# Kernel optimization log

Measured on AMD Instinct MI355X. Metric: run time of the kernel, lower is better.

Reference implementation:

```python
import jax, jax.numpy as jnp
import numpy as np

B, DIM, SEQ = 8, 256, 16384
K, RED = 3, 3
HID = DIM // RED          # 85
PAD, STRIDE = 1, 1
EPS = 1e-5                # BatchNorm eps (inference-mode BN with running stats)


def setup_inputs() -> dict:
    key = jax.random.key(0)
    ks = jax.random.split(key, 9)
    return {
        "x": jax.random.normal(ks[0], (B, DIM, SEQ), jnp.float32),
        "w1": jax.random.normal(ks[1], (HID, DIM), jnp.float32) * 0.05,
        "bn_gamma": jax.random.uniform(ks[2], (HID,), jnp.float32, 0.5, 1.5),
        "bn_beta": jax.random.normal(ks[3], (HID,), jnp.float32) * 0.1,
        "bn_mean": jax.random.normal(ks[4], (HID,), jnp.float32) * 0.1,
        "bn_var": jax.random.uniform(ks[5], (HID,), jnp.float32, 0.5, 1.5),
        "w2": jax.random.normal(ks[6], (DIM * K, HID), jnp.float32) * 0.05,
        "b2": jax.random.normal(ks[7], (DIM * K,), jnp.float32) * 0.05,
        "bias": jax.random.normal(ks[8], (DIM,), jnp.float32) * 0.05,
    }


def reference(x, w1, bn_gamma, bn_beta, bn_mean, bn_var, w2, b2, bias):
    b = x.shape[0]
    seq = x.shape[2]
    # squeeze: adaptive avg pool over seq -> [B, DIM]
    pooled = x.mean(axis=2)
    # conv1 (1x1, no bias) + inference BatchNorm + ReLU
    y = jnp.einsum('bc,hc->bh', pooled, w1)
    y = (y - bn_mean) * (bn_gamma * jax.lax.rsqrt(bn_var + EPS)) + bn_beta
    y = jax.nn.relu(y)
    # conv2 (1x1) -> per-sample depthwise kernels [B, DIM, K]
    w = (jnp.einsum('bh,oh->bo', y, w2) + b2).reshape(b, DIM, K)
    # dynamic depthwise conv1d (emulates F.conv1d with groups = B*DIM)
    xp = jnp.pad(x, ((0, 0), (0, 0), (PAD, PAD)))
    out_len = (seq + 2 * PAD - K) // STRIDE + 1
    out = jnp.zeros((b, DIM, out_len), x.dtype)
    for kk in range(K):  # small fixed kernel loop
        out = out + w[:, :, kk:kk + 1] * xp[:, :, kk:kk + out_len * STRIDE:STRIDE]
    return out + bias[None, :, None]
```

## Files before the change

kernel.cpp:

```cpp
#include <hip/hip_runtime.h>

#define B_      8
#define DIM_    256
#define SEQ_    16384
#define K_      3
#define HID_    85
#define OUTCH_  (DIM_ * K_)
#define EPS_    1e-5f

typedef float floatx4 __attribute__((ext_vector_type(4)));

__global__ __launch_bounds__(256) void pool_kernel(const float* __restrict__ x,
                                                   float* __restrict__ pooled) {
    const int row = blockIdx.x;
    const floatx4* x4 = (const floatx4*)(x + (size_t)row * SEQ_);
    float s = 0.f;
#pragma unroll
    for (int k = 0; k < SEQ_ / 4 / 256; ++k) {
        floatx4 v = x4[threadIdx.x + k * 256];
        s += (v.x + v.y) + (v.z + v.w);
    }
#pragma unroll
    for (int off = 32; off > 0; off >>= 1) s += __shfl_down(s, off, 64);
    __shared__ float lds[4];
    const int lane = threadIdx.x & 63, wid = threadIdx.x >> 6;
    if (lane == 0) lds[wid] = s;
    __syncthreads();
    if (threadIdx.x == 0) {
        float t = (lds[0] + lds[1]) + (lds[2] + lds[3]);
        pooled[row] = t * (1.0f / SEQ_);
    }
}

__global__ __launch_bounds__(256) void conv_kernel(const float* __restrict__ x,
                                                   const float* __restrict__ pooled,
                                                   const float* __restrict__ w1,
                                                   const float* __restrict__ gamma,
                                                   const float* __restrict__ beta,
                                                   const float* __restrict__ mean,
                                                   const float* __restrict__ var,
                                                   const float* __restrict__ w2,
                                                   const float* __restrict__ b2,
                                                   const float* __restrict__ bias,
                                                   float* __restrict__ out) {
    const int row = blockIdx.x;
    const int b = row >> 8;
    const int c = row & (DIM_ - 1);

    __shared__ float sp[DIM_];
    __shared__ float sy[HID_];
    sp[threadIdx.x] = pooled[b * DIM_ + threadIdx.x];
    __syncthreads();
    if (threadIdx.x < HID_) {
        const int h = threadIdx.x;
        const float* w1r = w1 + h * DIM_;
        float acc = 0.f;
#pragma unroll 8
        for (int cc = 0; cc < DIM_; ++cc) acc = fmaf(sp[cc], w1r[cc], acc);
        float t = (acc - mean[h]) * (gamma[h] * rsqrtf(var[h] + EPS_)) + beta[h];
        sy[h] = fmaxf(t, 0.f);
    }
    __syncthreads();

    const float* w2r0 = w2 + (c * 3 + 0) * HID_;
    const float* w2r1 = w2 + (c * 3 + 1) * HID_;
    const float* w2r2 = w2 + (c * 3 + 2) * HID_;
    float w0 = b2[c * 3 + 0], w1t = b2[c * 3 + 1], w2t = b2[c * 3 + 2];
    for (int h = 0; h < HID_; ++h) {
        const float yv = sy[h];
        w0  = fmaf(yv, w2r0[h], w0);
        w1t = fmaf(yv, w2r1[h], w1t);
        w2t = fmaf(yv, w2r2[h], w2t);
    }
    const float bs = bias[c];

    const float* xr = x + (size_t)row * SEQ_;
    const floatx4* x4 = (const floatx4*)xr;
    floatx4* o4 = (floatx4*)(out + (size_t)row * SEQ_);
    const int lane = threadIdx.x & 63;
#pragma unroll
    for (int k = 0; k < SEQ_ / 4 / 256; ++k) {
        const int j = threadIdx.x + k * 256;
        const int s0 = j * 4;
        floatx4 v = x4[j];
        float left  = __shfl_up(v.w, 1, 64);
        float right = __shfl_down(v.x, 1, 64);
        if (lane == 0)  left  = (s0 > 0)        ? xr[s0 - 1] : 0.f;
        if (lane == 63) right = (s0 + 4 < SEQ_) ? xr[s0 + 4] : 0.f;
        floatx4 r;
        r.x = fmaf(w0, left, fmaf(w1t, v.x, w2t * v.y)) + bs;
        r.y = fmaf(w0, v.x,  fmaf(w1t, v.y, w2t * v.z)) + bs;
        r.z = fmaf(w0, v.y,  fmaf(w1t, v.z, w2t * v.w)) + bs;
        r.w = fmaf(w0, v.z,  fmaf(w1t, v.w, w2t * right)) + bs;
        __builtin_nontemporal_store(r, &o4[j]);
    }
}

extern "C" void kernel_launch(void* const* d_in, const int* in_sizes, int n_in,
                              void* d_out, int out_size, void* d_ws, size_t ws_size,
                              hipStream_t stream) {
    const float* x     = (const float*)d_in[0];
    const float* w1    = (const float*)d_in[1];
    const float* gamma = (const float*)d_in[2];
    const float* beta  = (const float*)d_in[3];
    const float* mean  = (const float*)d_in[4];
    const float* var   = (const float*)d_in[5];
    const float* w2    = (const float*)d_in[6];
    const float* b2    = (const float*)d_in[7];
    const float* bias  = (const float*)d_in[8];
    float* out = (float*)d_out;

    float* pooled = (float*)d_ws;

    pool_kernel<<<B_ * DIM_, 256, 0, stream>>>(x, pooled);
    conv_kernel<<<B_ * DIM_, 256, 0, stream>>>(x, pooled, w1, gamma, beta, mean,
                                               var, w2, b2, bias, out);
}
```

Before: 292.8 us.

## Split per-sample MLP into its own kernel so conv blocks skip redundant matvecs

```diff
diff --git a/kernel.cpp b/kernel.cpp
--- a/kernel.cpp
+++ b/kernel.cpp
@@ -5,21 +5,23 @@
 #define SEQ_    16384
 #define K_      3
 #define HID_    85
-#define OUTCH_  (DIM_ * K_)
 #define EPS_    1e-5f
 
 typedef float floatx4 __attribute__((ext_vector_type(4)));
 
-__global__ __launch_bounds__(256) void pool_kernel(const float* __restrict__ x,
-                                                   float* __restrict__ pooled) {
+__global__ __launch_bounds__(256, 8) void pool_kernel(const float* __restrict__ x,
+                                                      float* __restrict__ pooled) {
     const int row = blockIdx.x;
     const floatx4* x4 = (const floatx4*)(x + (size_t)row * SEQ_);
-    float s = 0.f;
+    float s0 = 0.f, s1 = 0.f;
 #pragma unroll
-    for (int k = 0; k < SEQ_ / 4 / 256; ++k) {
-        floatx4 v = x4[threadIdx.x + k * 256];
-        s += (v.x + v.y) + (v.z + v.w);
+    for (int k = 0; k < SEQ_ / 4 / 256; k += 2) {
+        floatx4 a = x4[threadIdx.x + k * 256];
+        floatx4 b = x4[threadIdx.x + (k + 1) * 256];
+        s0 += (a.x + a.y) + (a.z + a.w);
+        s1 += (b.x + b.y) + (b.z + b.w);
     }
+    float s = s0 + s1;
 #pragma unroll
     for (int off = 32; off > 0; off >>= 1) s += __shfl_down(s, off, 64);
     __shared__ float lds[4];
@@ -32,21 +34,17 @@
     }
 }
 
-__global__ __launch_bounds__(256) void conv_kernel(const float* __restrict__ x,
-                                                   const float* __restrict__ pooled,
-                                                   const float* __restrict__ w1,
-                                                   const float* __restrict__ gamma,
-                                                   const float* __restrict__ beta,
-                                                   const float* __restrict__ mean,
-                                                   const float* __restrict__ var,
-                                                   const float* __restrict__ w2,
-                                                   const float* __restrict__ b2,
-                                                   const float* __restrict__ bias,
-                                                   float* __restrict__ out) {
-    const int row = blockIdx.x;
-    const int b = row >> 8;
-    const int c = row & (DIM_ - 1);
-
+__global__ __launch_bounds__(256) void mlp_kernel(const float* __restrict__ pooled,
+                                                  const float* __restrict__ w1,
+                                                  const float* __restrict__ gamma,
+                                                  const float* __restrict__ beta,
+                                                  const float* __restrict__ mean,
+                                                  const float* __restrict__ var,
+                                                  const float* __restrict__ w2,
+                                                  const float* __restrict__ b2,
+                                                  const float* __restrict__ bias,
+                                                  floatx4* __restrict__ taps) {
+    const int b = blockIdx.x;
     __shared__ float sp[DIM_];
     __shared__ float sy[HID_];
     sp[threadIdx.x] = pooled[b * DIM_ + threadIdx.x];
@@ -61,18 +59,29 @@
         sy[h] = fmaxf(t, 0.f);
     }
     __syncthreads();
-
+    const int c = threadIdx.x;
     const float* w2r0 = w2 + (c * 3 + 0) * HID_;
     const float* w2r1 = w2 + (c * 3 + 1) * HID_;
     const float* w2r2 = w2 + (c * 3 + 2) * HID_;
-    float w0 = b2[c * 3 + 0], w1t = b2[c * 3 + 1], w2t = b2[c * 3 + 2];
+    float t0 = b2[c * 3 + 0], t1 = b2[c * 3 + 1], t2 = b2[c * 3 + 2];
+#pragma unroll 5
     for (int h = 0; h < HID_; ++h) {
         const float yv = sy[h];
-        w0  = fmaf(yv, w2r0[h], w0);
-        w1t = fmaf(yv, w2r1[h], w1t);
-        w2t = fmaf(yv, w2r2[h], w2t);
+        t0 = fmaf(yv, w2r0[h], t0);
+        t1 = fmaf(yv, w2r1[h], t1);
+        t2 = fmaf(yv, w2r2[h], t2);
     }
-    const float bs = bias[c];
+    floatx4 t;
+    t.x = t0; t.y = t1; t.z = t2; t.w = bias[c];
+    taps[b * DIM_ + c] = t;
+}
+
+__global__ __launch_bounds__(256, 8) void conv_kernel(const float* __restrict__ x,
+                                                      const floatx4* __restrict__ taps,
+                                                      float* __restrict__ out) {
+    const int row = blockIdx.x;
+    const floatx4 t = taps[row];
+    const float w0 = t.x, w1t = t.y, w2t = t.z, bs = t.w;
 
     const float* xr = x + (size_t)row * SEQ_;
     const floatx4* x4 = (const floatx4*)xr;
@@ -111,8 +120,10 @@
     float* out = (float*)d_out;
 
     float* pooled = (float*)d_ws;
+    floatx4* taps = (floatx4*)((float*)d_ws + B_ * DIM_);
 
     pool_kernel<<<B_ * DIM_, 256, 0, stream>>>(x, pooled);
-    conv_kernel<<<B_ * DIM_, 256, 0, stream>>>(x, pooled, w1, gamma, beta, mean,
-                                               var, w2, b2, bias, out);
+    mlp_kernel<<<B_, 256, 0, stream>>>(pooled, w1, gamma, beta, mean, var,
+                                       w2, b2, bias, taps);
+    conv_kernel<<<B_ * DIM_, 256, 0, stream>>>(x, taps, out);
 }
```

After: 289.8 us. Within noise of the previous version (-1.0%).
